# Performance work log

Hardware: AMD Instinct MI355X
Metric: run time of the kernel (lower is better)

The kernel has to match this reference:

```python
import jax, jax.numpy as jnp
import numpy as np

B, N, D, H = 32, 512, 1024, 16
HD = D // H          # head_dim = 64
SEG = 64             # seg_num (router set size, softmax axis)
FACTOR = N           # einsum forces factor == seq_len


def setup_inputs() -> dict:
    key = jax.random.key(0)
    ks = jax.random.split(key, 12)
    s = 0.02
    return {
        "query": jax.random.normal(ks[0], (B, N, D), jnp.float32),
        "key":   jax.random.normal(ks[1], (B, N, D), jnp.float32),
        "value": jax.random.normal(ks[2], (B, N, D), jnp.float32),
        "router": jax.random.normal(ks[3], (SEG, FACTOR, HD), jnp.float32),
        "Wq": jax.random.normal(ks[4], (D, D), jnp.float32) * s,
        "bq": jnp.zeros((D,), jnp.float32),
        "Wk": jax.random.normal(ks[5], (D, D), jnp.float32) * s,
        "bk": jnp.zeros((D,), jnp.float32),
        "Wv": jax.random.normal(ks[6], (D, D), jnp.float32) * s,
        "bv": jnp.zeros((D,), jnp.float32),
        "Wo": jax.random.normal(ks[7], (D, D), jnp.float32) * s,
        "bo": jnp.zeros((D,), jnp.float32),
    }


def reference(query, key, value, router, Wq, bq, Wk, bk, Wv, bv, Wo, bo):
    b = query.shape[0]
    q = query @ Wq + bq                      # (B, N, D)
    k = key @ Wk + bk                        # computed but unused (faithful to source)
    v = value @ Wv + bv                      # computed but unused (faithful to source)
    # (B, N, H, HD) -> (B, H, N, HD)
    qh = q.reshape(b, -1, H, HD).transpose(0, 2, 1, 3)
    # torch: einsum('bnhd,bfhd->bnhf', q_bHnd, router_bSFd); shared 'h' = seq/factor
    # scores: (B, H, N, SEG); softmax over router/segment axis
    scores = jnp.einsum('bhnd,snd->bhns', qh, router)
    attn = jax.nn.softmax(scores, axis=-1)   # dropout = identity (eval mode)
    # combine: (B, H, N, HD)
    received = jnp.einsum('bhns,snd->bhnd', attn, router)
    received = received.transpose(0, 2, 1, 3).reshape(b, -1, D)
    output = received @ Wo + bo              # (B, N, D)
    return output, attn
```

## Files before the change

### kernel.cpp

```cpp
#include <hip/hip_runtime.h>

#define DEV __device__ __forceinline__

typedef __attribute__((ext_vector_type(8))) short bf16x8;
typedef __attribute__((ext_vector_type(4))) float f32x4;

constexpr int Bc  = 32;
constexpr int Nc  = 512;
constexpr int Dc  = 1024;
constexpr int Hc  = 16;
constexpr int HDc = 64;
constexpr int SEGc= 64;
constexpr int Mrows = Bc * Nc;

DEV unsigned short bf16r(float x) {
  union { float f; unsigned int u; } c; c.f = x;
  unsigned int r = (c.u + 0x7fffu + ((c.u >> 16) & 1u)) >> 16;
  return (unsigned short)r;
}

DEV void async_ld16(const void* g, void* l) {
  __builtin_amdgcn_global_load_lds(
      (const __attribute__((address_space(1))) void*)g,
      (__attribute__((address_space(3))) void*)l,
      16, 0, 0);
}

__global__ void cvt_bf16(const float* __restrict__ src,
                         unsigned short* __restrict__ dst, int n4) {
  int i = blockIdx.x * blockDim.x + threadIdx.x;
  if (i >= n4) return;
  float4 v = ((const float4*)src)[i];
  ushort4 o;
  o.x = bf16r(v.x); o.y = bf16r(v.y); o.z = bf16r(v.z); o.w = bf16r(v.w);
  ((ushort4*)dst)[i] = o;
}

__global__ void transpose_bf16(const float* __restrict__ src,
                               unsigned short* __restrict__ dst) {
  __shared__ float tile[32][33];
  int bx = blockIdx.x & 31, by = blockIdx.x >> 5;
  int tx = threadIdx.x & 31, ty = threadIdx.x >> 5;
  for (int i = 0; i < 4; ++i) {
    int r = ty + i * 8;
    tile[r][tx] = src[(size_t)(by * 32 + r) * 1024 + bx * 32 + tx];
  }
  __syncthreads();
  for (int i = 0; i < 4; ++i) {
    int r = ty + i * 8;
    dst[(size_t)(bx * 32 + r) * 1024 + by * 32 + tx] = bf16r(tile[tx][r]);
  }
}

template <bool OUT_F32>
__global__ __launch_bounds__(256)
void gemm_bt(const unsigned short* __restrict__ A,
             const unsigned short* __restrict__ BT,
             const float* __restrict__ bias,
             void* __restrict__ Cout) {
  constexpr int K = 1024, Nn = 1024, BM = 128, BN = 128, BK = 32;
  __shared__ unsigned short As[BM * BK];
  __shared__ unsigned short Bs[BN * BK];
  const int tid = threadIdx.x, lane = tid & 63, wave = tid >> 6;
  const int tm = blockIdx.x >> 3, tn = blockIdx.x & 7;
  const int wm = (wave >> 1) * 64, wn = (wave & 1) * 64;
  const int la = lane & 15, lb8 = (lane >> 4) * 8;

  f32x4 acc[4][4] = {};

  const int srow = tid >> 2;
  const int scol = (tid & 3) * 8;
  const unsigned short* Ag = A  + (size_t)(tm * BM + srow) * K + scol;
  const unsigned short* Bg = BT + (size_t)(tn * BN + srow) * K + scol;
  unsigned short* ldsA = As + wave * 512;
  unsigned short* ldsB = Bs + wave * 512;

  for (int k0 = 0; k0 < K; k0 += BK) {
    __syncthreads();
    async_ld16(Ag + k0,          ldsA);
    async_ld16(Ag + 64 * K + k0, ldsA + 2048);
    async_ld16(Bg + k0,          ldsB);
    async_ld16(Bg + 64 * K + k0, ldsB + 2048);
    __syncthreads();

    bf16x8 af[4], bfr[4];
#pragma unroll
    for (int i = 0; i < 4; ++i)
      af[i] = *(const bf16x8*)(As + (wm + i * 16 + la) * BK + lb8);
#pragma unroll
    for (int j = 0; j < 4; ++j)
      bfr[j] = *(const bf16x8*)(Bs + (wn + j * 16 + la) * BK + lb8);
#pragma unroll
    for (int i = 0; i < 4; ++i)
#pragma unroll
      for (int j = 0; j < 4; ++j)
        acc[i][j] = __builtin_amdgcn_mfma_f32_16x16x32_bf16(af[i], bfr[j],
                                                            acc[i][j], 0, 0, 0);
  }

  const int colbase = tn * BN + wn;
  float bv[4];
#pragma unroll
  for (int j = 0; j < 4; ++j) bv[j] = bias[colbase + j * 16 + la];
#pragma unroll
  for (int i = 0; i < 4; ++i) {
    int row0 = tm * BM + wm + i * 16 + (lane >> 4) * 4;
#pragma unroll
    for (int j = 0; j < 4; ++j) {
      int col = colbase + j * 16 + la;
#pragma unroll
      for (int r = 0; r < 4; ++r) {
        float v = acc[i][j][r] + bv[j];
        size_t idx = (size_t)(row0 + r) * Nn + col;
        if (OUT_F32) ((float*)Cout)[idx] = v;
        else         ((unsigned short*)Cout)[idx] = bf16r(v);
      }
    }
  }
}

__global__ __launch_bounds__(256)
void router_mid(const unsigned short* __restrict__ qb,
                const unsigned short* __restrict__ routerb,
                float* __restrict__ attn_out,
                unsigned short* __restrict__ recv_out) {
  __shared__ unsigned short Rs [SEGc * HDc];
  __shared__ unsigned short RTs[HDc * SEGc];
  __shared__ unsigned short AT [4 * 16 * 64];

  const int n = blockIdx.x;
  const int tid = threadIdx.x, lane = tid & 63, wave = tid >> 6;
  const int la = lane & 15, lb8 = (lane >> 4) * 8;

  {
    int s  = tid >> 3;
    int c8 = (tid & 7) * 8;
    async_ld16(routerb + ((size_t)s        * Nc + n) * HDc + c8, Rs + wave * 512);
    async_ld16(routerb + ((size_t)(s + 32) * Nc + n) * HDc + c8, Rs + 2048 + wave * 512);
  }
  __syncthreads();
  for (int i = 0; i < 16; ++i) {
    int idx = tid * 16 + i;
    RTs[(idx & 63) * 64 + (idx >> 6)] = Rs[idx];
  }
  __syncthreads();

  bf16x8 bs[4][2], br[4][2];
#pragma unroll
  for (int t = 0; t < 4; ++t)
#pragma unroll
    for (int kc = 0; kc < 2; ++kc) {
      bs[t][kc] = *(const bf16x8*)(Rs  + (t * 16 + la) * 64 + kc * 32 + lb8);
      br[t][kc] = *(const bf16x8*)(RTs + (t * 16 + la) * 64 + kc * 32 + lb8);
    }

  unsigned short* ATw = AT + wave * (16 * 64);

  for (int it = 0; it < 8; ++it) {
    const int bidx = wave * 8 + it;
    const unsigned short* qrow = qb + ((size_t)(bidx * Nc + n)) * Dc + la * 64;
    bf16x8 aq0 = *(const bf16x8*)(qrow + lb8);
    bf16x8 aq1 = *(const bf16x8*)(qrow + 32 + lb8);

    f32x4 sacc[4] = {};
#pragma unroll
    for (int t = 0; t < 4; ++t) {
      sacc[t] = __builtin_amdgcn_mfma_f32_16x16x32_bf16(aq0, bs[t][0], sacc[t], 0, 0, 0);
      sacc[t] = __builtin_amdgcn_mfma_f32_16x16x32_bf16(aq1, bs[t][1], sacc[t], 0, 0, 0);
    }

#pragma unroll
    for (int r = 0; r < 4; ++r) {
      float mx = fmaxf(fmaxf(sacc[0][r], sacc[1][r]), fmaxf(sacc[2][r], sacc[3][r]));
#pragma unroll
      for (int off = 1; off < 16; off <<= 1) mx = fmaxf(mx, __shfl_xor(mx, off));
      float e0 = __expf(sacc[0][r] - mx), e1 = __expf(sacc[1][r] - mx);
      float e2 = __expf(sacc[2][r] - mx), e3 = __expf(sacc[3][r] - mx);
      float sum = e0 + e1 + e2 + e3;
#pragma unroll
      for (int off = 1; off < 16; off <<= 1) sum += __shfl_xor(sum, off);
      float inv = 1.0f / sum;
      e0 *= inv; e1 *= inv; e2 *= inv; e3 *= inv;

      const int hrow = (lane >> 4) * 4 + r;
      const size_t m = (size_t)bidx * 16 + hrow;
      float* ao = attn_out + (m * Nc + n) * SEGc + la;
      ao[0] = e0; ao[16] = e1; ao[32] = e2; ao[48] = e3;
      unsigned short* aw = ATw + hrow * 64 + la;
      aw[0] = bf16r(e0); aw[16] = bf16r(e1); aw[32] = bf16r(e2); aw[48] = bf16r(e3);
    }

    __asm__ volatile("s_waitcnt lgkmcnt(0)" ::: "memory");
    bf16x8 ar0 = *(const bf16x8*)(ATw + la * 64 + lb8);
    bf16x8 ar1 = *(const bf16x8*)(ATw + la * 64 + 32 + lb8);

    f32x4 racc[4] = {};
#pragma unroll
    for (int t = 0; t < 4; ++t) {
      racc[t] = __builtin_amdgcn_mfma_f32_16x16x32_bf16(ar0, br[t][0], racc[t], 0, 0, 0);
      racc[t] = __builtin_amdgcn_mfma_f32_16x16x32_bf16(ar1, br[t][1], racc[t], 0, 0, 0);
    }

#pragma unroll
    for (int r = 0; r < 4; ++r) {
      const int h = (lane >> 4) * 4 + r;
      unsigned short* ro = recv_out + ((size_t)(bidx * Nc + n)) * Dc + h * 64 + la;
#pragma unroll
      for (int t = 0; t < 4; ++t) ro[t * 16] = bf16r(racc[t][r]);
    }
  }
}

extern "C" void kernel_launch(void* const* d_in, const int* in_sizes, int n_in,
                              void* d_out, int out_size, void* d_ws, size_t ws_size,
                              hipStream_t stream) {
  const float* query  = (const float*)d_in[0];
  const float* router = (const float*)d_in[3];
  const float* Wq     = (const float*)d_in[4];
  const float* bq     = (const float*)d_in[5];
  const float* Wo     = (const float*)d_in[10];
  const float* bo     = (const float*)d_in[11];

  float* out      = (float*)d_out;
  float* attn_out = out + (size_t)Bc * Nc * Dc;

  char* ws = (char*)d_ws;
  unsigned short* query_b  = (unsigned short*)(ws);
  unsigned short* q_b      = (unsigned short*)(ws + 33554432);
  unsigned short* recv_b   = (unsigned short*)(ws + 2u * 33554432);
  unsigned short* router_b = (unsigned short*)(ws + 3u * 33554432);
  unsigned short* WqT      = (unsigned short*)(ws + 3u * 33554432 + 4194304);
  unsigned short* WoT      = (unsigned short*)(ws + 3u * 33554432 + 4194304 + 2097152);

  cvt_bf16<<<16384, 256, 0, stream>>>(query,  query_b,  (Mrows * Dc) / 4);
  cvt_bf16<<<2048,  256, 0, stream>>>(router, router_b, (SEGc * Nc * HDc) / 4);
  transpose_bf16<<<1024, 256, 0, stream>>>(Wq, WqT);
  transpose_bf16<<<1024, 256, 0, stream>>>(Wo, WoT);

  gemm_bt<false><<<(Mrows / 128) * 8, 256, 0, stream>>>(query_b, WqT, bq, q_b);
  router_mid<<<Nc, 256, 0, stream>>>(q_b, router_b, attn_out, recv_b);
  gemm_bt<true ><<<(Mrows / 128) * 8, 256, 0, stream>>>(recv_b, WoT, bo, out);
}
```

Before: 400.8 us.

## Stage GEMM and router outputs through LDS for vectorized coalesced stores, double router grid

The GEMM epilogue now writes accumulators into the reused LDS tiles and then emits float4/ushort4 row-contiguous global stores in place of scattered scalar stores. The router kernel likewise stages its attention probabilities and received vectors in LDS, then writes them out as 16-byte coalesced stores. Its grid is also doubled so each block covers half the batch, which should improve occupancy. The cost is extra LDS traffic and barriers per epilogue row-tile, and the router tile is now loaded twice.

New measurement: 399.9 us. No clear change (-0.2%).

```diff
diff --git a/kernel.cpp b/kernel.cpp
--- a/kernel.cpp
+++ b/kernel.cpp
@@ -64,7 +64,7 @@
   const int tid = threadIdx.x, lane = tid & 63, wave = tid >> 6;
   const int tm = blockIdx.x >> 3, tn = blockIdx.x & 7;
   const int wm = (wave >> 1) * 64, wn = (wave & 1) * 64;
-  const int la = lane & 15, lb8 = (lane >> 4) * 8;
+  const int la = lane & 15, quad = lane >> 4, lb8 = quad * 8;
 
   f32x4 acc[4][4] = {};
 
@@ -102,18 +102,32 @@
   float bv[4];
 #pragma unroll
   for (int j = 0; j < 4; ++j) bv[j] = bias[colbase + j * 16 + la];
+
+  float* eps = (wave < 2) ? ((float*)As) + wave * 1024
+                          : ((float*)Bs) + (wave - 2) * 1024;
+  const int rowbase = tm * BM + wm;
+
 #pragma unroll
   for (int i = 0; i < 4; ++i) {
-    int row0 = tm * BM + wm + i * 16 + (lane >> 4) * 4;
-#pragma unroll
-    for (int j = 0; j < 4; ++j) {
-      int col = colbase + j * 16 + la;
-#pragma unroll
-      for (int r = 0; r < 4; ++r) {
-        float v = acc[i][j][r] + bv[j];
-        size_t idx = (size_t)(row0 + r) * Nn + col;
-        if (OUT_F32) ((float*)Cout)[idx] = v;
-        else         ((unsigned short*)Cout)[idx] = bf16r(v);
+    __syncthreads();
+#pragma unroll
+    for (int j = 0; j < 4; ++j)
+#pragma unroll
+      for (int r = 0; r < 4; ++r)
+        eps[(quad * 4 + r) * 64 + j * 16 + la] = acc[i][j][r] + bv[j];
+    __syncthreads();
+#pragma unroll
+    for (int s = 0; s < 4; ++s) {
+      int idx = s * 64 + lane;
+      int row = idx >> 4, c4 = idx & 15;
+      float4 v = *(const float4*)(eps + row * 64 + c4 * 4);
+      size_t goff = (size_t)(rowbase + i * 16 + row) * Nn + colbase + c4 * 4;
+      if (OUT_F32) {
+        *(float4*)((float*)Cout + goff) = v;
+      } else {
+        ushort4 u;
+        u.x = bf16r(v.x); u.y = bf16r(v.y); u.z = bf16r(v.z); u.w = bf16r(v.w);
+        *(ushort4*)((unsigned short*)Cout + goff) = u;
       }
     }
   }
@@ -127,14 +141,15 @@
   __shared__ unsigned short Rs [SEGc * HDc];
   __shared__ unsigned short RTs[HDc * SEGc];
   __shared__ unsigned short AT [4 * 16 * 64];
-
-  const int n = blockIdx.x;
+  __shared__ float          FW [4 * 16 * 64];
+
+  const int n = blockIdx.x >> 1, half = blockIdx.x & 1;
   const int tid = threadIdx.x, lane = tid & 63, wave = tid >> 6;
-  const int la = lane & 15, lb8 = (lane >> 4) * 8;
+  const int la = lane & 15, quad = lane >> 4, lb8 = quad * 8;
 
   {
+    int c8 = (tid & 7) * 8;
     int s  = tid >> 3;
-    int c8 = (tid & 7) * 8;
     async_ld16(routerb + ((size_t)s        * Nc + n) * HDc + c8, Rs + wave * 512);
     async_ld16(routerb + ((size_t)(s + 32) * Nc + n) * HDc + c8, Rs + 2048 + wave * 512);
   }
@@ -154,10 +169,11 @@
       br[t][kc] = *(const bf16x8*)(RTs + (t * 16 + la) * 64 + kc * 32 + lb8);
     }
 
-  unsigned short* ATw = AT + wave * (16 * 64);
-
-  for (int it = 0; it < 8; ++it) {
-    const int bidx = wave * 8 + it;
+  unsigned short* ATw = AT + wave * 1024;
+  float*          FWw = FW + wave * 1024;
+
+  for (int it = 0; it < 4; ++it) {
+    const int bidx = half * 16 + wave * 4 + it;
     const unsigned short* qrow = qb + ((size_t)(bidx * Nc + n)) * Dc + la * 64;
     bf16x8 aq0 = *(const bf16x8*)(qrow + lb8);
     bf16x8 aq1 = *(const bf16x8*)(qrow + 32 + lb8);
@@ -182,10 +198,9 @@
       float inv = 1.0f / sum;
       e0 *= inv; e1 *= inv; e2 *= inv; e3 *= inv;
 
-      const int hrow = (lane >> 4) * 4 + r;
-      const size_t m = (size_t)bidx * 16 + hrow;
-      float* ao = attn_out + (m * Nc + n) * SEGc + la;
-      ao[0] = e0; ao[16] = e1; ao[32] = e2; ao[48] = e3;
+      const int hrow = quad * 4 + r;
+      float* fw = FWw + hrow * 64 + la;
+      fw[0] = e0; fw[16] = e1; fw[32] = e2; fw[48] = e3;
       unsigned short* aw = ATw + hrow * 64 + la;
       aw[0] = bf16r(e0); aw[16] = bf16r(e1); aw[32] = bf16r(e2); aw[48] = bf16r(e3);
     }
@@ -202,12 +217,25 @@
     }
 
 #pragma unroll
+    for (int s = 0; s < 4; ++s) {
+      int idx = s * 64 + lane;
+      int row = idx >> 4, c4 = idx & 15;
+      float4 v = *(const float4*)(FWw + row * 64 + c4 * 4);
+      *(float4*)(attn_out + ((size_t)(bidx * 16 + row) * Nc + n) * SEGc + c4 * 4) = v;
+    }
+
+#pragma unroll
     for (int r = 0; r < 4; ++r) {
-      const int h = (lane >> 4) * 4 + r;
-      unsigned short* ro = recv_out + ((size_t)(bidx * Nc + n)) * Dc + h * 64 + la;
-#pragma unroll
-      for (int t = 0; t < 4; ++t) ro[t * 16] = bf16r(racc[t][r]);
-    }
+      const int h = quad * 4 + r;
+      unsigned short* aw = ATw + h * 64 + la;
+#pragma unroll
+      for (int t = 0; t < 4; ++t) aw[t * 16] = bf16r(racc[t][r]);
+    }
+    __asm__ volatile("s_waitcnt lgkmcnt(0)" ::: "memory");
+    unsigned short* ro = recv_out + ((size_t)(bidx * Nc + n)) * Dc;
+#pragma unroll
+    for (int s = 0; s < 2; ++s)
+      *(bf16x8*)(ro + s * 512 + lane * 8) = *(const bf16x8*)(ATw + s * 512 + lane * 8);
   }
 }
 
@@ -238,6 +266,6 @@
   transpose_bf16<<<1024, 256, 0, stream>>>(Wo, WoT);
 
   gemm_bt<false><<<(Mrows / 128) * 8, 256, 0, stream>>>(query_b, WqT, bq, q_b);
-  router_mid<<<Nc, 256, 0, stream>>>(q_b, router_b, attn_out, recv_b);
+  router_mid<<<2 * Nc, 256, 0, stream>>>(q_b, router_b, attn_out, recv_b);
   gemm_bt<true ><<<(Mrows / 128) * 8, 256, 0, stream>>>(recv_b, WoT, bo, out);
 }
```
